# Performance work log

Measured on AMD Instinct MI355X. Metric: run time of the kernel, lower is better.

Reference implementation:

```python
import jax, jax.numpy as jnp
import numpy as np


def setup_inputs() -> dict:
    key = jax.random.key(0)
    k1, k2, k3 = jax.random.split(key, 3)
    p = 4096
    target = jax.random.normal(k1, (p, p), dtype=jnp.float32)
    source = jax.random.normal(k2, (p, p), dtype=jnp.float32)
    W_beta = jax.random.uniform(k3, (p, p), dtype=jnp.float32)
    return {"target": target, "source": source, "W_beta": W_beta}


def reference(target, source, W_beta):
    # X = target, Y = source (module-level names in the original).
    # denominator inner loop: sum_i X[i] . X[i] == ||X||_F^2 (scalar),
    # recomputed p^2 times in the original; computed once here.
    s = jnp.sum(target * target)
    W = W_beta.sum(axis=1)                       # [p]
    W2 = W * W                                   # [p]
    scale = W2 / (s * W2 + 1.0)                  # [p]
    G = jnp.matmul(source, target.T)             # [p,p], G[i,j] = Y[i] . X[j]
    W_matrix = scale[:, None] * G                # [p,p]
    primary = jnp.matmul(W_matrix, target) - source
    loss = jnp.sqrt(jnp.sum(jnp.square(jnp.matmul(W_beta, primary))))
    return loss, W_matrix
```

## Files before the change

### kernel.cpp

```cpp
#include <hip/hip_runtime.h>
#include <hip/hip_bf16.h>

#define PDIM 4096
#define PPN ((size_t)PDIM * (size_t)PDIM)

typedef __attribute__((ext_vector_type(8))) short bf16x8;
typedef __attribute__((ext_vector_type(4))) float floatx4;
typedef __attribute__((ext_vector_type(8))) int int8v;

__device__ __forceinline__ void load_lds16(const void* g, void* l) {
  __builtin_amdgcn_global_load_lds(
      (const __attribute__((address_space(1))) void*)g,
      (__attribute__((address_space(3))) void*)l, 16, 0, 0);
}

__device__ __forceinline__ unsigned short bf16bits(float f) {
  __hip_bfloat16 h = __float2bfloat16(f);
  return *(unsigned short*)&h;
}

__device__ __forceinline__ unsigned char fp8byte(float v) {
  return (unsigned char)(__builtin_amdgcn_cvt_pk_fp8_f32(v, v, 0, false) & 0xff);
}
__device__ __forceinline__ unsigned int fp8x4(float a, float b, float c, float d) {
  int v = __builtin_amdgcn_cvt_pk_fp8_f32(a, b, 0, false);
  v = __builtin_amdgcn_cvt_pk_fp8_f32(c, d, v, true);
  return (unsigned int)v;
}

__global__ void sumsq(const float4* __restrict__ x, float* __restrict__ acc) {
  float s = 0.f;
  const size_t n4 = PPN / 4;
  for (size_t i = (size_t)blockIdx.x * 256 + threadIdx.x; i < n4;
       i += (size_t)gridDim.x * 256) {
    const float4 v = x[i];
    s += v.x * v.x + v.y * v.y + v.z * v.z + v.w * v.w;
  }
#pragma unroll
  for (int off = 32; off > 0; off >>= 1) s += __shfl_down(s, off);
  __shared__ float ws[4];
  if ((threadIdx.x & 63) == 0) ws[threadIdx.x >> 6] = s;
  __syncthreads();
  if (threadIdx.x == 0) atomicAdd(acc, ws[0] + ws[1] + ws[2] + ws[3]);
}

__global__ void cast_x(const float* __restrict__ src,
                       __hip_bfloat16* __restrict__ dstN,
                       unsigned char* __restrict__ dstT8) {
  __shared__ float tile[64][65];
  const int bx = blockIdx.x * 64, by = blockIdx.y * 64;
  const int tx = threadIdx.x & 15, ty = threadIdx.x >> 4;
#pragma unroll
  for (int r = 0; r < 4; ++r) {
    const int row = ty + r * 16;
    const float4 v = *(const float4*)&src[(size_t)(by + row) * PDIM + bx + tx * 4];
    tile[row][tx * 4 + 0] = v.x;
    tile[row][tx * 4 + 1] = v.y;
    tile[row][tx * 4 + 2] = v.z;
    tile[row][tx * 4 + 3] = v.w;
    ushort4 o;
    o.x = bf16bits(v.x); o.y = bf16bits(v.y); o.z = bf16bits(v.z); o.w = bf16bits(v.w);
    *(ushort4*)&dstN[(size_t)(by + row) * PDIM + bx + tx * 4] = o;
  }
  __syncthreads();
#pragma unroll
  for (int r = 0; r < 4; ++r) {
    const int i = ty + r * 16;
    *(unsigned int*)&dstT8[(size_t)(bx + i) * PDIM + by + tx * 4] =
        fp8x4(tile[tx * 4 + 0][i], tile[tx * 4 + 1][i],
              tile[tx * 4 + 2][i], tile[tx * 4 + 3][i]);
  }
}

__global__ void cast_y(const float* __restrict__ src,
                       __hip_bfloat16* __restrict__ dstN,
                       __hip_bfloat16* __restrict__ dstT) {
  __shared__ float tile[64][65];
  const int bx = blockIdx.x * 64, by = blockIdx.y * 64;
  const int tx = threadIdx.x & 15, ty = threadIdx.x >> 4;
#pragma unroll
  for (int r = 0; r < 4; ++r) {
    const int row = ty + r * 16;
    const float4 v = *(const float4*)&src[(size_t)(by + row) * PDIM + bx + tx * 4];
    tile[row][tx * 4 + 0] = v.x;
    tile[row][tx * 4 + 1] = v.y;
    tile[row][tx * 4 + 2] = v.z;
    tile[row][tx * 4 + 3] = v.w;
    ushort4 o;
    o.x = bf16bits(v.x); o.y = bf16bits(v.y); o.z = bf16bits(v.z); o.w = bf16bits(v.w);
    *(ushort4*)&dstN[(size_t)(by + row) * PDIM + bx + tx * 4] = o;
  }
  __syncthreads();
#pragma unroll
  for (int r = 0; r < 4; ++r) {
    const int i = ty + r * 16;
    ushort4 o;
    o.x = bf16bits(tile[tx * 4 + 0][i]);
    o.y = bf16bits(tile[tx * 4 + 1][i]);
    o.z = bf16bits(tile[tx * 4 + 2][i]);
    o.w = bf16bits(tile[tx * 4 + 3][i]);
    *(ushort4*)&dstT[(size_t)(bx + i) * PDIM + by + tx * 4] = o;
  }
}

__global__ void cast_wb_rows(const float* __restrict__ Wb,
                             unsigned char* __restrict__ Wb8,
                             const float* __restrict__ sAcc,
                             float* __restrict__ scale) {
  const size_t row = blockIdx.x;
  const float4* src = (const float4*)(Wb + row * PDIM);
  unsigned int* dst = (unsigned int*)(Wb8 + row * PDIM);
  float sum = 0.f;
#pragma unroll
  for (int it = 0; it < 4; ++it) {
    const int j = threadIdx.x + it * 256;
    const float4 v = src[j];
    sum += (v.x + v.y) + (v.z + v.w);
    dst[j] = fp8x4(v.x, v.y, v.z, v.w);
  }
#pragma unroll
  for (int off = 32; off > 0; off >>= 1) sum += __shfl_down(sum, off);
  __shared__ float ws[4];
  if ((threadIdx.x & 63) == 0) ws[threadIdx.x >> 6] = sum;
  __syncthreads();
  if (threadIdx.x == 0) {
    const float W = ws[0] + ws[1] + ws[2] + ws[3];
    const float w2 = W * W;
    scale[row] = w2 / ((*sAcc) * w2 + 1.0f);
  }
}

__global__ __launch_bounds__(256)
void gemm_bf16_wm(const __hip_bfloat16* __restrict__ A,
                  const __hip_bfloat16* __restrict__ B,
                  const float* __restrict__ scale,
                  float* __restrict__ outF,
                  unsigned char* __restrict__ Wm8) {
  __shared__ __align__(16) __hip_bfloat16 As[128 * 32];
  __shared__ __align__(16) __hip_bfloat16 Bs[128 * 32];

  const int tid = threadIdx.x;
  const int lane = tid & 63;
  const int wave = tid >> 6;
  const int wm = wave >> 1, wn = wave & 1;

  const size_t rowA0 = (size_t)blockIdx.y * 128;
  const size_t rowB0 = (size_t)blockIdx.x * 128;

  const int c0 = tid, c1 = tid + 256;
  const int r0 = c0 >> 2, r1 = c1 >> 2;
  const int sc0 = (c0 & 3) ^ ((r0 >> 1) & 3);
  const int sc1 = (c1 & 3) ^ ((r1 >> 1) & 3);
  const __hip_bfloat16* gA0 = A + (rowA0 + (size_t)r0) * PDIM + sc0 * 8;
  const __hip_bfloat16* gA1 = A + (rowA0 + (size_t)r1) * PDIM + sc1 * 8;
  const __hip_bfloat16* gB0 = B + (rowB0 + (size_t)r0) * PDIM + sc0 * 8;
  const __hip_bfloat16* gB1 = B + (rowB0 + (size_t)r1) * PDIM + sc1 * 8;

  char* ldsA0 = (char*)As + wave * 1024;
  char* ldsA1 = (char*)As + 4096 + wave * 1024;
  char* ldsB0 = (char*)Bs + wave * 1024;
  char* ldsB1 = (char*)Bs + 4096 + wave * 1024;

  floatx4 acc[4][4] = {};

  const int fr = lane & 15;
  const int kq = lane >> 4;
  const int sw = (fr >> 1) & 3;
  const int ko = (kq ^ sw) * 16;

  for (int kt = 0; kt < PDIM; kt += 32) {
    load_lds16(gA0 + kt, ldsA0);
    load_lds16(gA1 + kt, ldsA1);
    load_lds16(gB0 + kt, ldsB0);
    load_lds16(gB1 + kt, ldsB1);
    __syncthreads();

    bf16x8 af[4], bfr[4];
#pragma unroll
    for (int mi = 0; mi < 4; ++mi)
      af[mi] = *(const bf16x8*)((const char*)As + (wm * 64 + mi * 16 + fr) * 64 + ko);
#pragma unroll
    for (int ni = 0; ni < 4; ++ni)
      bfr[ni] = *(const bf16x8*)((const char*)Bs + (wn * 64 + ni * 16 + fr) * 64 + ko);
#pragma unroll
    for (int mi = 0; mi < 4; ++mi)
#pragma unroll
      for (int ni = 0; ni < 4; ++ni)
        acc[mi][ni] = __builtin_amdgcn_mfma_f32_16x16x32_bf16(
            af[mi], bfr[ni], acc[mi][ni], 0, 0, 0);
    __syncthreads();
  }

  const size_t row0 = rowA0 + wm * 64;
  const size_t col0 = rowB0 + wn * 64;
  const int lr = (lane >> 4) << 2;
  const int lc = lane & 15;

#pragma unroll
  for (int mi = 0; mi < 4; ++mi) {
#pragma unroll
    for (int r = 0; r < 4; ++r) {
      const size_t row = row0 + mi * 16 + lr + r;
      const float sc = scale[row];
#pragma unroll
      for (int ni = 0; ni < 4; ++ni) {
        const size_t col = col0 + ni * 16 + lc;
        const float v = sc * acc[mi][ni][r];
        outF[row * PDIM + col] = v;
        Wm8[row * PDIM + col] = fp8byte(v * 131072.f);
      }
    }
  }
}

template <int MODE>
__global__ __launch_bounds__(256)
void gemm_fp8(const unsigned char* __restrict__ A,
              const unsigned char* __restrict__ B,
              const __hip_bfloat16* __restrict__ sub,
              unsigned char* __restrict__ outP,
              float* __restrict__ lossAcc) {
  __shared__ __align__(16) unsigned char As[128 * 128];
  __shared__ __align__(16) unsigned char Bs[128 * 128];

  const int tid = threadIdx.x;
  const int lane = tid & 63;
  const int wave = tid >> 6;
  const int wm = wave >> 1, wn = wave & 1;

  const size_t rowA0 = (size_t)blockIdx.y * 128;
  const size_t rowB0 = (size_t)blockIdx.x * 128;

  const unsigned char* gA[4];
  const unsigned char* gB[4];
  int ldsOff[4];
#pragma unroll
  for (int m = 0; m < 4; ++m) {
    const int ci = tid + m * 256;
    const int r = ci >> 3, s = ci & 7;
    const int cg = s ^ (r & 7);
    gA[m] = A + (rowA0 + (size_t)r) * PDIM + cg * 16;
    gB[m] = B + (rowB0 + (size_t)r) * PDIM + cg * 16;
    ldsOff[m] = m * 4096 + wave * 1024;
  }

  floatx4 acc[4][4] = {};

  const int fr = lane & 15;
  const int e = fr & 7;
  const int q2 = (lane >> 4) << 1;
  const int offLo = (q2 ^ e) << 4;
  const int offHi = ((q2 + 1) ^ e) << 4;
  const int abase = (wm * 64 + fr) * 128;
  const int bbase = (wn * 64 + fr) * 128;

  for (int kt = 0; kt < PDIM; kt += 128) {
#pragma unroll
    for (int m = 0; m < 4; ++m) load_lds16(gA[m] + kt, (char*)As + ldsOff[m]);
#pragma unroll
    for (int m = 0; m < 4; ++m) load_lds16(gB[m] + kt, (char*)Bs + ldsOff[m]);
    __syncthreads();

    union { int8v v; int4 h[2]; } af[4], bg[4];
#pragma unroll
    for (int mi = 0; mi < 4; ++mi) {
      af[mi].h[0] = *(const int4*)(As + abase + mi * 2048 + offLo);
      af[mi].h[1] = *(const int4*)(As + abase + mi * 2048 + offHi);
    }
#pragma unroll
    for (int ni = 0; ni < 4; ++ni) {
      bg[ni].h[0] = *(const int4*)(Bs + bbase + ni * 2048 + offLo);
      bg[ni].h[1] = *(const int4*)(Bs + bbase + ni * 2048 + offHi);
    }
#pragma unroll
    for (int mi = 0; mi < 4; ++mi)
#pragma unroll
      for (int ni = 0; ni < 4; ++ni)
        acc[mi][ni] = __builtin_amdgcn_mfma_scale_f32_16x16x128_f8f6f4(
            af[mi].v, bg[ni].v, acc[mi][ni],
            0 , 0 , 0, 0x7F7F7F7F, 0, 0x7F7F7F7F);
    __syncthreads();
  }

  const size_t row0 = rowA0 + wm * 64;
  const size_t col0 = rowB0 + wn * 64;
  const int lr = (lane >> 4) << 2;
  const int lc = lane & 15;

  if constexpr (MODE == 2) {
    float tot = 0.f;
#pragma unroll
    for (int mi = 0; mi < 4; ++mi)
#pragma unroll
      for (int ni = 0; ni < 4; ++ni)
#pragma unroll
        for (int r = 0; r < 4; ++r) tot += acc[mi][ni][r] * acc[mi][ni][r];
#pragma unroll
    for (int off = 32; off > 0; off >>= 1) tot += __shfl_down(tot, off);
    __shared__ float ws[4];
    if (lane == 0) ws[wave] = tot;
    __syncthreads();
    if (tid == 0) atomicAdd(lossAcc, ws[0] + ws[1] + ws[2] + ws[3]);
  } else {
    constexpr float INV = 1.f / 131072.f;
#pragma unroll
    for (int mi = 0; mi < 4; ++mi) {
#pragma unroll
      for (int r = 0; r < 4; ++r) {
        const size_t row = row0 + mi * 16 + lr + r;
#pragma unroll
        for (int ni = 0; ni < 4; ++ni) {
          const size_t col = col0 + ni * 16 + lc;
          const float v = acc[mi][ni][r] * INV - __bfloat162float(sub[row * PDIM + col]);
          outP[row * PDIM + col] = fp8byte(v);
        }
      }
    }
  }
}

__global__ void finalize(float* __restrict__ out, const float* __restrict__ acc) {
  if (threadIdx.x == 0) out[0] = sqrtf(*acc);
}

extern "C" void kernel_launch(void* const* d_in, const int* in_sizes, int n_in,
                              void* d_out, int out_size, void* d_ws, size_t ws_size,
                              hipStream_t stream) {
  const float* X  = (const float*)d_in[0];
  const float* Y  = (const float*)d_in[1];
  const float* Wb = (const float*)d_in[2];
  float* out = (float*)d_out;

  __hip_bfloat16* Xb   = (__hip_bfloat16*)d_ws;
  __hip_bfloat16* Yb   = Xb + PPN;
  __hip_bfloat16* YbT  = Yb + PPN;
  unsigned char*  XT8  = (unsigned char*)(YbT + PPN);
  unsigned char*  Wm8  = XT8 + PPN;
  unsigned char*  Wb8  = Wm8 + PPN;
  unsigned char*  PT8  = Wb8 + PPN;
  float* scale   = (float*)(PT8 + PPN);
  float* sAcc    = scale + PDIM;
  float* lossAcc = sAcc + 1;

  hipMemsetAsync(sAcc, 0, 2 * sizeof(float), stream);

  sumsq<<<1024, 256, 0, stream>>>((const float4*)X, sAcc);

  dim3 cgrid(PDIM / 64, PDIM / 64);
  cast_x<<<cgrid, 256, 0, stream>>>(X, Xb, XT8);
  cast_y<<<cgrid, 256, 0, stream>>>(Y, Yb, YbT);
  cast_wb_rows<<<PDIM, 256, 0, stream>>>(Wb, Wb8, sAcc, scale);

  dim3 ggrid(PDIM / 128, PDIM / 128);
  gemm_bf16_wm<<<ggrid, 256, 0, stream>>>(Yb, Xb, scale, out + 1, Wm8);
  gemm_fp8<1><<<ggrid, 256, 0, stream>>>(XT8, Wm8, YbT, PT8, nullptr);
  gemm_fp8<2><<<ggrid, 256, 0, stream>>>(PT8, Wb8, nullptr, nullptr, lossAcc);

  finalize<<<1, 1, 0, stream>>>(out, lossAcc);
}
```

Baseline: 606.2 us.

## Rewrite bf16 GEMM as 256x256-tile, 8-wave, double-buffered ping-pong pipeline

Replaces the 128x128, 4-wave, single-buffered bf16 GEMM that feeds W_matrix with a 256x256-tile, 512-thread kernel. It uses a K-step of 64 and 128 KB of double-buffered LDS, with async global-to-LDS loads issued two tiles ahead. The MFMA work is split into four quadrants with s_setprio and barriers so loads overlap compute, and a block-index swizzle is added for L2 locality. This aims to raise MFMA utilisation and cut LDS/global traffic per flop, at the cost of heavy LDS use (one block per CU), hand-tuned waitcnt logic that could hide races, and only 256 blocks across the GPU.

```diff
diff --git a/kernel.cpp b/kernel.cpp
--- a/kernel.cpp
+++ b/kernel.cpp
@@ -130,81 +130,158 @@
   }
 }
 
-__global__ __launch_bounds__(256)
+__device__ __forceinline__ void mfma_quad(floatx4 (&acc)[8][4], int mo, int no,
+                                          const bf16x8 (&af)[8],
+                                          const bf16x8 (&bf)[4]) {
+  __builtin_amdgcn_s_setprio(1);
+#pragma unroll
+  for (int mi = 0; mi < 4; ++mi)
+#pragma unroll
+    for (int ni = 0; ni < 2; ++ni)
+#pragma unroll
+      for (int kk = 0; kk < 2; ++kk)
+        acc[mo + mi][no + ni] = __builtin_amdgcn_mfma_f32_16x16x32_bf16(
+            af[mi * 2 + kk], bf[ni * 2 + kk], acc[mo + mi][no + ni], 0, 0, 0);
+  __builtin_amdgcn_s_setprio(0);
+}
+
+__global__ __launch_bounds__(512, 2)
 void gemm_bf16_wm(const __hip_bfloat16* __restrict__ A,
                   const __hip_bfloat16* __restrict__ B,
                   const float* __restrict__ scale,
                   float* __restrict__ outF,
                   unsigned char* __restrict__ Wm8) {
-  __shared__ __align__(16) __hip_bfloat16 As[128 * 32];
-  __shared__ __align__(16) __hip_bfloat16 Bs[128 * 32];
+  __shared__ __align__(16) char LDS[131072];
 
   const int tid = threadIdx.x;
   const int lane = tid & 63;
   const int wave = tid >> 6;
-  const int wm = wave >> 1, wn = wave & 1;
-
-  const size_t rowA0 = (size_t)blockIdx.y * 128;
-  const size_t rowB0 = (size_t)blockIdx.x * 128;
-
-  const int c0 = tid, c1 = tid + 256;
-  const int r0 = c0 >> 2, r1 = c1 >> 2;
-  const int sc0 = (c0 & 3) ^ ((r0 >> 1) & 3);
-  const int sc1 = (c1 & 3) ^ ((r1 >> 1) & 3);
-  const __hip_bfloat16* gA0 = A + (rowA0 + (size_t)r0) * PDIM + sc0 * 8;
-  const __hip_bfloat16* gA1 = A + (rowA0 + (size_t)r1) * PDIM + sc1 * 8;
-  const __hip_bfloat16* gB0 = B + (rowB0 + (size_t)r0) * PDIM + sc0 * 8;
-  const __hip_bfloat16* gB1 = B + (rowB0 + (size_t)r1) * PDIM + sc1 * 8;
-
-  char* ldsA0 = (char*)As + wave * 1024;
-  char* ldsA1 = (char*)As + 4096 + wave * 1024;
-  char* ldsB0 = (char*)Bs + wave * 1024;
-  char* ldsB1 = (char*)Bs + 4096 + wave * 1024;
-
-  floatx4 acc[4][4] = {};
+  const int wm = wave >> 2;
+  const int wn = wave & 3;
+
+  const int bid = blockIdx.x;
+  const int swz = (bid & 7) * 32 + (bid >> 3);
+  const int bx = swz & 15;
+  const int by = swz >> 4;
+  const size_t rowA0 = (size_t)by * 256;
+  const size_t rowB0 = (size_t)bx * 256;
+
+  const int srow = tid >> 3;
+  const int scol = ((tid & 7) ^ (srow & 7)) << 4;
+  const char* pA = (const char*)A + (rowA0 + srow) * 8192 + scol;
+  const char* pB = (const char*)B + (rowB0 + srow) * 8192 + scol;
+  const int ldsWav = wave * 1024;
 
   const int fr = lane & 15;
   const int kq = lane >> 4;
-  const int sw = (fr >> 1) & 3;
-  const int ko = (kq ^ sw) * 16;
-
-  for (int kt = 0; kt < PDIM; kt += 32) {
-    load_lds16(gA0 + kt, ldsA0);
-    load_lds16(gA1 + kt, ldsA1);
-    load_lds16(gB0 + kt, ldsB0);
-    load_lds16(gB1 + kt, ldsB1);
-    __syncthreads();
-
-    bf16x8 af[4], bfr[4];
-#pragma unroll
-    for (int mi = 0; mi < 4; ++mi)
-      af[mi] = *(const bf16x8*)((const char*)As + (wm * 64 + mi * 16 + fr) * 64 + ko);
-#pragma unroll
-    for (int ni = 0; ni < 4; ++ni)
-      bfr[ni] = *(const bf16x8*)((const char*)Bs + (wn * 64 + ni * 16 + fr) * 64 + ko);
-#pragma unroll
-    for (int mi = 0; mi < 4; ++mi)
-#pragma unroll
-      for (int ni = 0; ni < 4; ++ni)
-        acc[mi][ni] = __builtin_amdgcn_mfma_f32_16x16x32_bf16(
-            af[mi], bfr[ni], acc[mi][ni], 0, 0, 0);
-    __syncthreads();
-  }
-
-  const size_t row0 = rowA0 + wm * 64;
-  const size_t col0 = rowB0 + wn * 64;
+  const int slot0 = ((kq ^ (fr & 7)) << 4);
+  const int aRowB = (wm * 64 + fr) * 128;
+  const int bRowB = (wn * 32 + fr) * 128;
+
+  floatx4 acc[8][4] = {};
+  bf16x8 af[8], bLo[4], bHi[4];
+
+  {
+    char* dA0 = LDS + ldsWav;
+    char* dB0 = LDS + 65536 + ldsWav;
+    load_lds16(pA, dA0);
+    load_lds16(pA + 524288, dA0 + 8192);
+    load_lds16(pB, dB0);
+    load_lds16(pB + 524288, dB0 + 8192);
+    load_lds16(pB + 1048576, dB0 + 16384);
+    load_lds16(pB + 1048576 + 524288, dB0 + 16384 + 8192);
+    load_lds16(pA + 1048576, dA0 + 16384);
+    load_lds16(pA + 1048576 + 524288, dA0 + 16384 + 8192);
+    char* dA1 = dA0 + 32768;
+    char* dB1 = dB0 + 32768;
+    load_lds16(pA + 128, dA1);
+    load_lds16(pA + 128 + 524288, dA1 + 8192);
+    load_lds16(pB + 128, dB1);
+    load_lds16(pB + 128 + 524288, dB1 + 8192);
+    load_lds16(pB + 128 + 1048576, dB1 + 16384);
+    load_lds16(pB + 128 + 1048576 + 524288, dB1 + 16384 + 8192);
+    load_lds16(pA + 128 + 1048576, dA1 + 16384);
+    load_lds16(pA + 128 + 1048576 + 524288, dA1 + 16384 + 8192);
+  }
+  asm volatile("s_waitcnt vmcnt(8)" ::: "memory");
+  __builtin_amdgcn_s_barrier();
+
+  for (int t = 0; t < 64; ++t) {
+    const int buf = (t & 1) << 15;
+    const int tS = (t + 2) & 63;
+    const char* sA = pA + (size_t)tS * 128;
+    const char* sB = pB + (size_t)tS * 128;
+    char* dA = LDS + buf + ldsWav;
+    char* dB = LDS + 65536 + buf + ldsWav;
+    const char* aRd = LDS + buf + aRowB;
+    const char* bRd = LDS + 65536 + buf + bRowB;
+
+#pragma unroll
+    for (int mi = 0; mi < 4; ++mi) {
+      af[mi * 2 + 0] = *(const bf16x8*)(aRd + mi * 2048 + slot0);
+      af[mi * 2 + 1] = *(const bf16x8*)(aRd + mi * 2048 + (slot0 ^ 64));
+    }
+#pragma unroll
+    for (int ni = 0; ni < 2; ++ni) {
+      bLo[ni * 2 + 0] = *(const bf16x8*)(bRd + ni * 2048 + slot0);
+      bLo[ni * 2 + 1] = *(const bf16x8*)(bRd + ni * 2048 + (slot0 ^ 64));
+    }
+    load_lds16(sA, dA);
+    load_lds16(sA + 524288, dA + 8192);
+    asm volatile("s_waitcnt lgkmcnt(8)" ::: "memory");
+    __builtin_amdgcn_s_barrier();
+    asm volatile("s_waitcnt lgkmcnt(0)" ::: "memory");
+    __builtin_amdgcn_sched_barrier(0);
+    mfma_quad(acc, 0, 0, af, bLo);
+    __builtin_amdgcn_s_barrier();
+
+#pragma unroll
+    for (int ni = 0; ni < 2; ++ni) {
+      bHi[ni * 2 + 0] = *(const bf16x8*)(bRd + 16384 + ni * 2048 + slot0);
+      bHi[ni * 2 + 1] = *(const bf16x8*)(bRd + 16384 + ni * 2048 + (slot0 ^ 64));
+    }
+    load_lds16(sB, dB);
+    load_lds16(sB + 524288, dB + 8192);
+    __builtin_amdgcn_s_barrier();
+    asm volatile("s_waitcnt lgkmcnt(0)" ::: "memory");
+    __builtin_amdgcn_sched_barrier(0);
+    mfma_quad(acc, 0, 2, af, bHi);
+    __builtin_amdgcn_s_barrier();
+
+#pragma unroll
+    for (int mi = 0; mi < 4; ++mi) {
+      af[mi * 2 + 0] = *(const bf16x8*)(aRd + 16384 + mi * 2048 + slot0);
+      af[mi * 2 + 1] = *(const bf16x8*)(aRd + 16384 + mi * 2048 + (slot0 ^ 64));
+    }
+    load_lds16(sB + 1048576, dB + 16384);
+    load_lds16(sB + 1048576 + 524288, dB + 16384 + 8192);
+    __builtin_amdgcn_s_barrier();
+    asm volatile("s_waitcnt lgkmcnt(0)" ::: "memory");
+    __builtin_amdgcn_sched_barrier(0);
+    mfma_quad(acc, 4, 2, af, bHi);
+    __builtin_amdgcn_s_barrier();
+
+    asm volatile("s_waitcnt vmcnt(6)" ::: "memory");
+    __builtin_amdgcn_sched_barrier(0);
+    load_lds16(sA + 1048576, dA + 16384);
+    load_lds16(sA + 1048576 + 524288, dA + 16384 + 8192);
+    __builtin_amdgcn_s_barrier();
+    mfma_quad(acc, 4, 0, af, bLo);
+    __builtin_amdgcn_s_barrier();
+  }
+
   const int lr = (lane >> 4) << 2;
   const int lc = lane & 15;
-
-#pragma unroll
-  for (int mi = 0; mi < 4; ++mi) {
+#pragma unroll
+  for (int mi = 0; mi < 8; ++mi) {
+    const size_t rbase = rowA0 + (size_t)(mi >> 2) * 128 + wm * 64 + (mi & 3) * 16 + lr;
 #pragma unroll
     for (int r = 0; r < 4; ++r) {
-      const size_t row = row0 + mi * 16 + lr + r;
+      const size_t row = rbase + r;
       const float sc = scale[row];
 #pragma unroll
       for (int ni = 0; ni < 4; ++ni) {
-        const size_t col = col0 + ni * 16 + lc;
+        const size_t col = rowB0 + (size_t)(ni >> 1) * 128 + wn * 32 + (ni & 1) * 16 + lc;
         const float v = sc * acc[mi][ni][r];
         outF[row * PDIM + col] = v;
         Wm8[row * PDIM + col] = fp8byte(v * 131072.f);
@@ -351,8 +428,9 @@
   cast_y<<<cgrid, 256, 0, stream>>>(Y, Yb, YbT);
   cast_wb_rows<<<PDIM, 256, 0, stream>>>(Wb, Wb8, sAcc, scale);
 
+  gemm_bf16_wm<<<dim3(256), 512, 0, stream>>>(Yb, Xb, scale, out + 1, Wm8);
+
   dim3 ggrid(PDIM / 128, PDIM / 128);
-  gemm_bf16_wm<<<ggrid, 256, 0, stream>>>(Yb, Xb, scale, out + 1, Wm8);
   gemm_fp8<1><<<ggrid, 256, 0, stream>>>(XT8, Wm8, YbT, PT8, nullptr);
   gemm_fp8<2><<<ggrid, 256, 0, stream>>>(PT8, Wb8, nullptr, nullptr, lossAcc);
 
```

After: 541.0 us. -10.8%, faster.
